# Optimization experiments

Hardware: AMD Instinct MI355X
Metric: run time of the kernel (lower is better)

Reference implementation:

```python
import jax, jax.numpy as jnp
import numpy as np

Q, C, D = 4096, 4096, 1024
EPS = 1e-6  # torch.nn.PairwiseDistance default eps, added to (x1 - x2)


def _cdist_l2(a, b):
    # ||(a + EPS) - b||_2 for all pairs, via GEMM formulation.
    a = a + EPS
    sq = (jnp.sum(a * a, axis=1)[:, None]
          + jnp.sum(b * b, axis=1)[None, :]
          - 2.0 * a @ b.T)
    return jnp.sqrt(jnp.maximum(sq, 0.0))


def setup_inputs() -> dict:
    key = jax.random.key(0)
    k1, k2, k3, k4, k5, k6 = jax.random.split(key, 6)
    return {
        "context_rgb_features": jax.random.normal(k1, (C, D), dtype=jnp.float32),
        "context_flow_features": jax.random.normal(k2, (C, D), dtype=jnp.float32),
        "target_rgb_features": jax.random.normal(k3, (Q, D), dtype=jnp.float32),
        "target_flow_features": jax.random.normal(k4, (Q, D), dtype=jnp.float32),
        "c_r": jax.random.uniform(k5, (Q,), dtype=jnp.float32, minval=0.1, maxval=1.0),
        "c_f": jax.random.uniform(k6, (Q,), dtype=jnp.float32, minval=0.1, maxval=1.0),
    }


def reference(context_rgb_features, context_flow_features,
              target_rgb_features, target_flow_features, c_r, c_f):
    denom = c_r + c_f
    w_r = (c_r / denom)[:, None]   # [Q, 1]
    w_f = (c_f / denom)[:, None]
    d_rgb = _cdist_l2(target_rgb_features, context_rgb_features)    # [Q, C]
    d_flow = _cdist_l2(target_flow_features, context_flow_features)  # [Q, C]
    posterior = w_r * jnp.exp(-d_rgb) + w_f * jnp.exp(-d_flow)
    return posterior / jnp.sum(posterior, axis=1, keepdims=True)
```

## Files before the change

### kernel.cpp

```cpp
#include <hip/hip_runtime.h>
#include <hip/hip_bf16.h>

#define QN 4096
#define CN 4096
#define DN 1024
#define EPSV 1e-6f

#define BM 128
#define BN 128
#define BK 64
#define TILE (BM * BK)

#define MATSZ ((size_t)QN * DN)

using bf16x8 = __attribute__((ext_vector_type(8))) __bf16;
using f32x4  = __attribute__((ext_vector_type(4))) float;

static __device__ __forceinline__ unsigned short f2bf_rne(float x) {
  unsigned int u = __float_as_uint(x);
  unsigned int r = (u + 0x7FFFu + ((u >> 16) & 1u)) >> 16;
  return (unsigned short)r;
}
static __device__ __forceinline__ float bf2f(unsigned short h) {
  return __uint_as_float(((unsigned int)h) << 16);
}

static __device__ __forceinline__ void gload_lds16(const unsigned short* g, unsigned short* l) {
  __builtin_amdgcn_global_load_lds(
      (const __attribute__((address_space(1))) unsigned int*)g,
      (__attribute__((address_space(3))) unsigned int*)l, 16, 0, 0);
}


__global__ void prep_kernel(const float* __restrict__ tgt_r, const float* __restrict__ tgt_f,
                            const float* __restrict__ ctx_r, const float* __restrict__ ctx_f,
                            unsigned short* __restrict__ ws16, float* __restrict__ norms) {
  const int row = blockIdx.x;
  const int mat = blockIdx.y;
  const int t = threadIdx.x;
  const float* src; float eps;
  switch (mat) {
    case 0:  src = tgt_r; eps = EPSV; break;
    case 1:  src = tgt_f; eps = EPSV; break;
    case 2:  src = ctx_r; eps = 0.f;  break;
    default: src = ctx_f; eps = 0.f;  break;
  }
  unsigned short* hi = ws16 + (size_t)mat * MATSZ;
  float* nrm = norms + (size_t)mat * QN;
  const size_t base = (size_t)row * DN;
  float4 v = ((const float4*)(src + base))[t];
  float a[4] = {v.x + eps, v.y + eps, v.z + eps, v.w + eps};
  float ss = 0.f;
  unsigned short hh[4];
#pragma unroll
  for (int k = 0; k < 4; ++k) {
    hh[k] = f2bf_rne(a[k]);
    float f = bf2f(hh[k]);
    ss += f * f;
  }
  ((ushort4*)(hi + base))[t] = make_ushort4(hh[0], hh[1], hh[2], hh[3]);

#pragma unroll
  for (int o = 32; o > 0; o >>= 1) ss += __shfl_down(ss, o);
  __shared__ float red[4];
  if ((t & 63) == 0) red[t >> 6] = ss;
  __syncthreads();
  if (t == 0) nrm[row] = red[0] + red[1] + red[2] + red[3];
}

template <bool ACCUM>
__global__ __launch_bounds__(256, 3)
void gemm_kernel(const unsigned short* __restrict__ A,
                 const unsigned short* __restrict__ B,
                 const float* __restrict__ tn,
                 const float* __restrict__ cn,
                 const float* __restrict__ cw_num,
                 const float* __restrict__ cw_oth,
                 float* __restrict__ out) {
  __shared__ unsigned short S[2 * TILE];

  const int t = threadIdx.x;
  const int lane = t & 63;
  const int wid = t >> 6;
  const int wr = wid >> 1;
  const int wc = wid & 1;
  const int row0 = blockIdx.y * BM;
  const int col0 = blockIdx.x * BN;

  f32x4 acc[4][4];
#pragma unroll
  for (int i = 0; i < 4; ++i)
#pragma unroll
    for (int j = 0; j < 4; ++j)
      acc[i][j] = (f32x4){0.f, 0.f, 0.f, 0.f};

  const int srw = lane >> 3;
  const int sch = (lane & 7) ^ srw;
  const size_t src_off = (size_t)(wid * 8 + srw) * DN + sch * 8;
  const size_t aoff = (size_t)row0 * DN + src_off;
  const size_t boff = (size_t)col0 * DN + src_off;
  unsigned short* ldsW = S + wid * 8 * BK;

  const unsigned short* pA = A + aoff;
  const unsigned short* pB = B + boff;

  const int lr = lane & 15;
  const int lq = lane >> 4;
  const int sc0 = (lq ^ (lr & 7)) * 8;
  int ra[4], rb[4];
#pragma unroll
  for (int i = 0; i < 4; ++i) {
    ra[i] = (wr * 64 + i * 16 + lr) * BK + sc0;
    rb[i] = (wc * 64 + i * 16 + lr) * BK + sc0;
  }
#define KS1(x) ((x) ^ 32)

  for (int kc = 0; kc < DN / BK; ++kc) {
    const int k = kc * BK;
    __syncthreads();
#pragma unroll
    for (int it = 0; it < 4; ++it) {
      const size_t g = (size_t)it * 32 * DN + k;
      unsigned short* l = ldsW + it * 32 * BK;
      gload_lds16(pA + g, l + 0 * TILE);
      gload_lds16(pB + g, l + 1 * TILE);
    }
    __syncthreads();

#pragma unroll
    for (int ksub = 0; ksub < 2; ++ksub) {
      bf16x8 ar[4], br[4];
#pragma unroll
      for (int i = 0; i < 4; ++i) {
        const int oa = ksub ? KS1(ra[i]) : ra[i];
        const int ob = ksub ? KS1(rb[i]) : rb[i];
        ar[i] = *(const bf16x8*)(S + oa);
        br[i] = *(const bf16x8*)(S + TILE + ob);
      }
#pragma unroll
      for (int i = 0; i < 4; ++i)
#pragma unroll
        for (int j = 0; j < 4; ++j)
          acc[i][j] = __builtin_amdgcn_mfma_f32_16x16x32_bf16(ar[i], br[j], acc[i][j], 0, 0, 0);
    }
  }

  float cnv[4];
  int ccv[4];
#pragma unroll
  for (int j = 0; j < 4; ++j) {
    ccv[j] = col0 + wc * 64 + j * 16 + lr;
    cnv[j] = cn[ccv[j]];
  }

#pragma unroll
  for (int i = 0; i < 4; ++i) {
#pragma unroll
    for (int r = 0; r < 4; ++r) {
      const int tq = row0 + wr * 64 + i * 16 + lq * 4 + r;
      const float tnq = tn[tq];
      const float num = cw_num[tq], oth = cw_oth[tq];
      const float wgt = num / (num + oth);
      float* orow = out + (size_t)tq * CN;
#pragma unroll
      for (int j = 0; j < 4; ++j) {
        const float sq = tnq + cnv[j] - 2.f * acc[i][j][r];
        const float d = sqrtf(fmaxf(sq, 0.f));
        const float e = wgt * __expf(-d);
        if (ACCUM) {
          orow[ccv[j]] += e;
        } else {
          orow[ccv[j]] = e;
        }
      }
    }
  }
}

__global__ void norm_kernel(float* __restrict__ out) {
  const int row = blockIdx.x;
  const int t = threadIdx.x;
  float4* p = (float4*)(out + (size_t)row * CN);
  float4 v[4];
  float s = 0.f;
#pragma unroll
  for (int i = 0; i < 4; ++i) {
    v[i] = p[t + 256 * i];
    s += v[i].x + v[i].y + v[i].z + v[i].w;
  }
#pragma unroll
  for (int o = 32; o > 0; o >>= 1) s += __shfl_down(s, o);
  __shared__ float red[4];
  if ((t & 63) == 0) red[t >> 6] = s;
  __syncthreads();
  const float inv = 1.f / (red[0] + red[1] + red[2] + red[3]);
#pragma unroll
  for (int i = 0; i < 4; ++i) {
    v[i].x *= inv; v[i].y *= inv; v[i].z *= inv; v[i].w *= inv;
    p[t + 256 * i] = v[i];
  }
}

extern "C" void kernel_launch(void* const* d_in, const int* in_sizes, int n_in,
                              void* d_out, int out_size, void* d_ws, size_t ws_size,
                              hipStream_t stream) {
  const float* ctx_r = (const float*)d_in[0];
  const float* ctx_f = (const float*)d_in[1];
  const float* tgt_r = (const float*)d_in[2];
  const float* tgt_f = (const float*)d_in[3];
  const float* c_r   = (const float*)d_in[4];
  const float* c_f   = (const float*)d_in[5];
  float* out = (float*)d_out;
  unsigned short* ws16 = (unsigned short*)d_ws;
  float* norms = (float*)(ws16 + 4 * MATSZ);

  prep_kernel<<<dim3(QN, 4), 256, 0, stream>>>(tgt_r, tgt_f, ctx_r, ctx_f, ws16, norms);
  gemm_kernel<false><<<dim3(CN / BN, QN / BM), 256, 0, stream>>>(
      ws16 + 0 * MATSZ, ws16 + 2 * MATSZ, norms, norms + 2 * QN, c_r, c_f, out);
  gemm_kernel<true><<<dim3(CN / BN, QN / BM), 256, 0, stream>>>(
      ws16 + 1 * MATSZ, ws16 + 3 * MATSZ, norms + QN, norms + 3 * QN, c_f, c_r, out);
  norm_kernel<<<QN, 256, 0, stream>>>(out);
}
```

Measured before the change: 226.5 us.

## Fuse RGB and flow GEMMs into one kernel with LDS-staged coalesced epilogue

The two separate GEMM launches (RGB, then flow with read-modify-write accumulation into the output) become one kernel that loads all four bf16 operand tiles and keeps two accumulator sets. The combined posterior is written once, which removes the second kernel's read of the output matrix. The epilogue stages results through LDS so each row segment is stored as contiguous float4 writes. The prep and norm kernels now give one wavefront per row and drop the shared-memory reductions. The cost is double the accumulator registers and LDS, and occupancy drops from 3 to 2 blocks per CU.

```diff
diff --git a/kernel.cpp b/kernel.cpp
--- a/kernel.cpp
+++ b/kernel.cpp
@@ -12,6 +12,7 @@
 #define TILE (BM * BK)
 
 #define MATSZ ((size_t)QN * DN)
+#define SFP 132
 
 using bf16x8 = __attribute__((ext_vector_type(8))) __bf16;
 using f32x4  = __attribute__((ext_vector_type(4))) float;
@@ -35,9 +36,11 @@
 __global__ void prep_kernel(const float* __restrict__ tgt_r, const float* __restrict__ tgt_f,
                             const float* __restrict__ ctx_r, const float* __restrict__ ctx_f,
                             unsigned short* __restrict__ ws16, float* __restrict__ norms) {
-  const int row = blockIdx.x;
+  const int t = threadIdx.x;
+  const int w = t >> 6;
+  const int lane = t & 63;
+  const int row = blockIdx.x * 4 + w;
   const int mat = blockIdx.y;
-  const int t = threadIdx.x;
   const float* src; float eps;
   switch (mat) {
     case 0:  src = tgt_r; eps = EPSV; break;
@@ -48,36 +51,33 @@
   unsigned short* hi = ws16 + (size_t)mat * MATSZ;
   float* nrm = norms + (size_t)mat * QN;
   const size_t base = (size_t)row * DN;
-  float4 v = ((const float4*)(src + base))[t];
-  float a[4] = {v.x + eps, v.y + eps, v.z + eps, v.w + eps};
+  const float4* s4 = (const float4*)(src + base);
+  ushort4* d4 = (ushort4*)(hi + base);
   float ss = 0.f;
-  unsigned short hh[4];
-#pragma unroll
-  for (int k = 0; k < 4; ++k) {
-    hh[k] = f2bf_rne(a[k]);
-    float f = bf2f(hh[k]);
-    ss += f * f;
-  }
-  ((ushort4*)(hi + base))[t] = make_ushort4(hh[0], hh[1], hh[2], hh[3]);
-
+#pragma unroll
+  for (int i = 0; i < 4; ++i) {
+    float4 v = s4[lane + 64 * i];
+    float a[4] = {v.x + eps, v.y + eps, v.z + eps, v.w + eps};
+    unsigned short hh[4];
+#pragma unroll
+    for (int k = 0; k < 4; ++k) {
+      hh[k] = f2bf_rne(a[k]);
+      float f = bf2f(hh[k]);
+      ss += f * f;
+    }
+    d4[lane + 64 * i] = make_ushort4(hh[0], hh[1], hh[2], hh[3]);
+  }
 #pragma unroll
   for (int o = 32; o > 0; o >>= 1) ss += __shfl_down(ss, o);
-  __shared__ float red[4];
-  if ((t & 63) == 0) red[t >> 6] = ss;
-  __syncthreads();
-  if (t == 0) nrm[row] = red[0] + red[1] + red[2] + red[3];
-}
-
-template <bool ACCUM>
-__global__ __launch_bounds__(256, 3)
-void gemm_kernel(const unsigned short* __restrict__ A,
-                 const unsigned short* __restrict__ B,
-                 const float* __restrict__ tn,
-                 const float* __restrict__ cn,
-                 const float* __restrict__ cw_num,
-                 const float* __restrict__ cw_oth,
+  if (lane == 0) nrm[row] = ss;
+}
+
+__global__ __launch_bounds__(256, 2)
+void gemm_kernel(const unsigned short* __restrict__ ws16,
+                 const float* __restrict__ norms,
+                 const float* __restrict__ c_r, const float* __restrict__ c_f,
                  float* __restrict__ out) {
-  __shared__ unsigned short S[2 * TILE];
+  __shared__ unsigned short S[4 * TILE];
 
   const int t = threadIdx.x;
   const int lane = t & 63;
@@ -87,12 +87,14 @@
   const int row0 = blockIdx.y * BM;
   const int col0 = blockIdx.x * BN;
 
-  f32x4 acc[4][4];
-#pragma unroll
-  for (int i = 0; i < 4; ++i)
-#pragma unroll
-    for (int j = 0; j < 4; ++j)
-      acc[i][j] = (f32x4){0.f, 0.f, 0.f, 0.f};
+  f32x4 acc[2][4][4];
+#pragma unroll
+  for (int m = 0; m < 2; ++m)
+#pragma unroll
+    for (int i = 0; i < 4; ++i)
+#pragma unroll
+      for (int j = 0; j < 4; ++j)
+        acc[m][i][j] = (f32x4){0.f, 0.f, 0.f, 0.f};
 
   const int srw = lane >> 3;
   const int sch = (lane & 7) ^ srw;
@@ -101,8 +103,10 @@
   const size_t boff = (size_t)col0 * DN + src_off;
   unsigned short* ldsW = S + wid * 8 * BK;
 
-  const unsigned short* pA = A + aoff;
-  const unsigned short* pB = B + boff;
+  const unsigned short* pAr = ws16 + 0 * MATSZ + aoff;
+  const unsigned short* pAf = ws16 + 1 * MATSZ + aoff;
+  const unsigned short* pBr = ws16 + 2 * MATSZ + boff;
+  const unsigned short* pBf = ws16 + 3 * MATSZ + boff;
 
   const int lr = lane & 15;
   const int lq = lane >> 4;
@@ -122,82 +126,107 @@
     for (int it = 0; it < 4; ++it) {
       const size_t g = (size_t)it * 32 * DN + k;
       unsigned short* l = ldsW + it * 32 * BK;
-      gload_lds16(pA + g, l + 0 * TILE);
-      gload_lds16(pB + g, l + 1 * TILE);
+      gload_lds16(pAr + g, l + 0 * TILE);
+      gload_lds16(pAf + g, l + 1 * TILE);
+      gload_lds16(pBr + g, l + 2 * TILE);
+      gload_lds16(pBf + g, l + 3 * TILE);
     }
     __syncthreads();
 
 #pragma unroll
     for (int ksub = 0; ksub < 2; ++ksub) {
-      bf16x8 ar[4], br[4];
+      bf16x8 ar[4], af[4], br[4], bf[4];
 #pragma unroll
       for (int i = 0; i < 4; ++i) {
         const int oa = ksub ? KS1(ra[i]) : ra[i];
         const int ob = ksub ? KS1(rb[i]) : rb[i];
-        ar[i] = *(const bf16x8*)(S + oa);
-        br[i] = *(const bf16x8*)(S + TILE + ob);
+        ar[i] = *(const bf16x8*)(S + 0 * TILE + oa);
+        af[i] = *(const bf16x8*)(S + 1 * TILE + oa);
+        br[i] = *(const bf16x8*)(S + 2 * TILE + ob);
+        bf[i] = *(const bf16x8*)(S + 3 * TILE + ob);
       }
 #pragma unroll
       for (int i = 0; i < 4; ++i)
 #pragma unroll
-        for (int j = 0; j < 4; ++j)
-          acc[i][j] = __builtin_amdgcn_mfma_f32_16x16x32_bf16(ar[i], br[j], acc[i][j], 0, 0, 0);
-    }
-  }
-
-  float cnv[4];
-  int ccv[4];
+        for (int j = 0; j < 4; ++j) {
+          acc[0][i][j] = __builtin_amdgcn_mfma_f32_16x16x32_bf16(ar[i], br[j], acc[0][i][j], 0, 0, 0);
+          acc[1][i][j] = __builtin_amdgcn_mfma_f32_16x16x32_bf16(af[i], bf[j], acc[1][i][j], 0, 0, 0);
+        }
+    }
+  }
+
+  const float* tn_r = norms;
+  const float* tn_f = norms + QN;
+  const float* cn_r = norms + 2 * QN;
+  const float* cn_f = norms + 3 * QN;
+
+  float cnr[4], cnf[4];
 #pragma unroll
   for (int j = 0; j < 4; ++j) {
-    ccv[j] = col0 + wc * 64 + j * 16 + lr;
-    cnv[j] = cn[ccv[j]];
-  }
+    const int cc = col0 + wc * 64 + j * 16 + lr;
+    cnr[j] = cn_r[cc];
+    cnf[j] = cn_f[cc];
+  }
+
+  float* Sf = (float*)S;
+  const int lrow = t >> 3;
+  const int c0 = (t & 7) * 16;
+  const int grow_base = row0 + (lrow >> 4) * 64 + (lrow & 15);
+
+  __syncthreads();
 
 #pragma unroll
   for (int i = 0; i < 4; ++i) {
+    if (i > 0) __syncthreads();
 #pragma unroll
     for (int r = 0; r < 4; ++r) {
       const int tq = row0 + wr * 64 + i * 16 + lq * 4 + r;
-      const float tnq = tn[tq];
-      const float num = cw_num[tq], oth = cw_oth[tq];
-      const float wgt = num / (num + oth);
-      float* orow = out + (size_t)tq * CN;
+      const float tnr = tn_r[tq];
+      const float tnf = tn_f[tq];
+      const float cr = c_r[tq], cf = c_f[tq];
+      const float inv = 1.f / (cr + cf);
+      const float wgr = cr * inv, wgf = cf * inv;
+      float* sfrow = Sf + (wr * 16 + lq * 4 + r) * SFP + wc * 64 + lr;
 #pragma unroll
       for (int j = 0; j < 4; ++j) {
-        const float sq = tnq + cnv[j] - 2.f * acc[i][j][r];
-        const float d = sqrtf(fmaxf(sq, 0.f));
-        const float e = wgt * __expf(-d);
-        if (ACCUM) {
-          orow[ccv[j]] += e;
-        } else {
-          orow[ccv[j]] = e;
-        }
+        const float sr_ = tnr + cnr[j] - 2.f * acc[0][i][j][r];
+        const float sf_ = tnf + cnf[j] - 2.f * acc[1][i][j][r];
+        const float dr = sqrtf(fmaxf(sr_, 0.f));
+        const float df = sqrtf(fmaxf(sf_, 0.f));
+        sfrow[j * 16] = wgr * __expf(-dr) + wgf * __expf(-df);
       }
     }
+    __syncthreads();
+    const float* src = Sf + lrow * SFP + c0;
+    float4 v0 = ((const float4*)src)[0];
+    float4 v1 = ((const float4*)src)[1];
+    float4 v2 = ((const float4*)src)[2];
+    float4 v3 = ((const float4*)src)[3];
+    float4* dst = (float4*)(out + (size_t)(grow_base + i * 16) * CN + col0 + c0);
+    dst[0] = v0; dst[1] = v1; dst[2] = v2; dst[3] = v3;
   }
 }
 
 __global__ void norm_kernel(float* __restrict__ out) {
-  const int row = blockIdx.x;
   const int t = threadIdx.x;
+  const int w = t >> 6;
+  const int lane = t & 63;
+  const int row = blockIdx.x * 4 + w;
   float4* p = (float4*)(out + (size_t)row * CN);
-  float4 v[4];
+  float4 v[16];
   float s = 0.f;
 #pragma unroll
-  for (int i = 0; i < 4; ++i) {
-    v[i] = p[t + 256 * i];
+  for (int i = 0; i < 16; ++i) {
+    v[i] = p[lane + 64 * i];
     s += v[i].x + v[i].y + v[i].z + v[i].w;
   }
 #pragma unroll
   for (int o = 32; o > 0; o >>= 1) s += __shfl_down(s, o);
-  __shared__ float red[4];
-  if ((t & 63) == 0) red[t >> 6] = s;
-  __syncthreads();
-  const float inv = 1.f / (red[0] + red[1] + red[2] + red[3]);
-#pragma unroll
-  for (int i = 0; i < 4; ++i) {
+  const float inv = 1.f / __shfl(s, 0);
+#pragma unroll
+  for (int i = 0; i < 16; ++i) {
     v[i].x *= inv; v[i].y *= inv; v[i].z *= inv; v[i].w *= inv;
-    p[t + 256 * i] = v[i];
+    p[lane + 64 * i] = v[i];
   }
 }
 
@@ -214,10 +243,7 @@
   unsigned short* ws16 = (unsigned short*)d_ws;
   float* norms = (float*)(ws16 + 4 * MATSZ);
 
-  prep_kernel<<<dim3(QN, 4), 256, 0, stream>>>(tgt_r, tgt_f, ctx_r, ctx_f, ws16, norms);
-  gemm_kernel<false><<<dim3(CN / BN, QN / BM), 256, 0, stream>>>(
-      ws16 + 0 * MATSZ, ws16 + 2 * MATSZ, norms, norms + 2 * QN, c_r, c_f, out);
-  gemm_kernel<true><<<dim3(CN / BN, QN / BM), 256, 0, stream>>>(
-      ws16 + 1 * MATSZ, ws16 + 3 * MATSZ, norms + QN, norms + 3 * QN, c_f, c_r, out);
-  norm_kernel<<<QN, 256, 0, stream>>>(out);
-}
+  prep_kernel<<<dim3(QN / 4, 4), 256, 0, stream>>>(tgt_r, tgt_f, ctx_r, ctx_f, ws16, norms);
+  gemm_kernel<<<dim3(CN / BN, QN / BM), 256, 0, stream>>>(ws16, norms, c_r, c_f, out);
+  norm_kernel<<<QN / 4, 256, 0, stream>>>(out);
+}
```

New measurement: 236.0 us. +4.2%, slower.

## Fuse rgb and flow GEMMs into one double-buffered kernel

Applied to the files above, without the earlier changes.

Merges the two separate distance GEMM launches into a single kernel that accumulates both the rgb and flow products per output tile and writes the combined posterior once. This removes the read-modify-write pass over the output from the second GEMM and one launch. The main loop is restructured to a K=32 tile with double-buffered LDS staging, so the next tile loads while the current one computes. The cost is twice the accumulator registers, with launch bounds lowered to 2 blocks per CU, which reduces occupancy.

```diff
diff --git a/kernel.cpp b/kernel.cpp
--- a/kernel.cpp
+++ b/kernel.cpp
@@ -8,8 +8,9 @@
 
 #define BM 128
 #define BN 128
-#define BK 64
-#define TILE (BM * BK)
+#define TK 32
+#define TILEK (BM * TK)
+#define NT (DN / TK)
 
 #define MATSZ ((size_t)QN * DN)
 
@@ -59,7 +60,6 @@
     ss += f * f;
   }
   ((ushort4*)(hi + base))[t] = make_ushort4(hh[0], hh[1], hh[2], hh[3]);
-
 #pragma unroll
   for (int o = 32; o > 0; o >>= 1) ss += __shfl_down(ss, o);
   __shared__ float red[4];
@@ -68,16 +68,12 @@
   if (t == 0) nrm[row] = red[0] + red[1] + red[2] + red[3];
 }
 
-template <bool ACCUM>
-__global__ __launch_bounds__(256, 3)
-void gemm_kernel(const unsigned short* __restrict__ A,
-                 const unsigned short* __restrict__ B,
-                 const float* __restrict__ tn,
-                 const float* __restrict__ cn,
-                 const float* __restrict__ cw_num,
-                 const float* __restrict__ cw_oth,
+__global__ __launch_bounds__(256, 2)
+void gemm_kernel(const unsigned short* __restrict__ ws16,
+                 const float* __restrict__ norms,
+                 const float* __restrict__ c_r, const float* __restrict__ c_f,
                  float* __restrict__ out) {
-  __shared__ unsigned short S[2 * TILE];
+  __shared__ unsigned short S[2 * 4 * TILEK];
 
   const int t = threadIdx.x;
   const int lane = t & 63;
@@ -87,91 +83,102 @@
   const int row0 = blockIdx.y * BM;
   const int col0 = blockIdx.x * BN;
 
-  f32x4 acc[4][4];
-#pragma unroll
-  for (int i = 0; i < 4; ++i)
-#pragma unroll
-    for (int j = 0; j < 4; ++j)
-      acc[i][j] = (f32x4){0.f, 0.f, 0.f, 0.f};
-
-  const int srw = lane >> 3;
-  const int sch = (lane & 7) ^ srw;
-  const size_t src_off = (size_t)(wid * 8 + srw) * DN + sch * 8;
-  const size_t aoff = (size_t)row0 * DN + src_off;
-  const size_t boff = (size_t)col0 * DN + src_off;
-  unsigned short* ldsW = S + wid * 8 * BK;
-
-  const unsigned short* pA = A + aoff;
-  const unsigned short* pB = B + boff;
+  f32x4 acc[2][4][4];
+#pragma unroll
+  for (int m = 0; m < 2; ++m)
+#pragma unroll
+    for (int i = 0; i < 4; ++i)
+#pragma unroll
+      for (int j = 0; j < 4; ++j)
+        acc[m][i][j] = (f32x4){0.f, 0.f, 0.f, 0.f};
+
+  const int sch = ((lane & 3) ^ ((lane >> 3) & 3)) * 8;
+  const int r0 = wid * 16 + (lane >> 2);
+  const size_t sr0 = (size_t)r0 * DN + sch;
+  const size_t sr1 = (size_t)(r0 + 64) * DN + sch;
+  const int ldsb0 = (wid * 64) * 8;
+  const int ldsb1 = (256 + wid * 64) * 8;
+
+  const unsigned short* pAr = ws16 + 0 * MATSZ + (size_t)row0 * DN;
+  const unsigned short* pAf = ws16 + 1 * MATSZ + (size_t)row0 * DN;
+  const unsigned short* pBr = ws16 + 2 * MATSZ + (size_t)col0 * DN;
+  const unsigned short* pBf = ws16 + 3 * MATSZ + (size_t)col0 * DN;
 
   const int lr = lane & 15;
   const int lq = lane >> 4;
-  const int sc0 = (lq ^ (lr & 7)) * 8;
+  const int fch = (lq ^ ((lr >> 1) & 3)) * 8;
   int ra[4], rb[4];
 #pragma unroll
   for (int i = 0; i < 4; ++i) {
-    ra[i] = (wr * 64 + i * 16 + lr) * BK + sc0;
-    rb[i] = (wc * 64 + i * 16 + lr) * BK + sc0;
-  }
-#define KS1(x) ((x) ^ 32)
-
-  for (int kc = 0; kc < DN / BK; ++kc) {
-    const int k = kc * BK;
+    ra[i] = (wr * 64 + i * 16 + lr) * TK + fch;
+    rb[i] = (wc * 64 + i * 16 + lr) * TK + fch;
+  }
+
+#define STAGE(buf, kk)                                                        \
+  do {                                                                        \
+    unsigned short* Sb_ = S + (buf) * 4 * TILEK;                              \
+    gload_lds16(pAr + (kk) + sr0, Sb_ + 0 * TILEK + ldsb0);                   \
+    gload_lds16(pAr + (kk) + sr1, Sb_ + 0 * TILEK + ldsb1);                   \
+    gload_lds16(pAf + (kk) + sr0, Sb_ + 1 * TILEK + ldsb0);                   \
+    gload_lds16(pAf + (kk) + sr1, Sb_ + 1 * TILEK + ldsb1);                   \
+    gload_lds16(pBr + (kk) + sr0, Sb_ + 2 * TILEK + ldsb0);                   \
+    gload_lds16(pBr + (kk) + sr1, Sb_ + 2 * TILEK + ldsb1);                   \
+    gload_lds16(pBf + (kk) + sr0, Sb_ + 3 * TILEK + ldsb0);                   \
+    gload_lds16(pBf + (kk) + sr1, Sb_ + 3 * TILEK + ldsb1);                   \
+  } while (0)
+
+  STAGE(0, 0);
+  __syncthreads();
+
+  int cur = 0;
+  for (int tt = 0; tt < NT; ++tt) {
+    if (tt + 1 < NT) STAGE(cur ^ 1, (tt + 1) * TK);
+
+    const unsigned short* Sb = S + cur * 4 * TILEK;
+    bf16x8 ar[4], af[4], br[4], bf[4];
+#pragma unroll
+    for (int i = 0; i < 4; ++i) {
+      ar[i] = *(const bf16x8*)(Sb + 0 * TILEK + ra[i]);
+      af[i] = *(const bf16x8*)(Sb + 1 * TILEK + ra[i]);
+      br[i] = *(const bf16x8*)(Sb + 2 * TILEK + rb[i]);
+      bf[i] = *(const bf16x8*)(Sb + 3 * TILEK + rb[i]);
+    }
+#pragma unroll
+    for (int i = 0; i < 4; ++i)
+#pragma unroll
+      for (int j = 0; j < 4; ++j) {
+        acc[0][i][j] = __builtin_amdgcn_mfma_f32_16x16x32_bf16(ar[i], br[j], acc[0][i][j], 0, 0, 0);
+        acc[1][i][j] = __builtin_amdgcn_mfma_f32_16x16x32_bf16(af[i], bf[j], acc[1][i][j], 0, 0, 0);
+      }
+
     __syncthreads();
-#pragma unroll
-    for (int it = 0; it < 4; ++it) {
-      const size_t g = (size_t)it * 32 * DN + k;
-      unsigned short* l = ldsW + it * 32 * BK;
-      gload_lds16(pA + g, l + 0 * TILE);
-      gload_lds16(pB + g, l + 1 * TILE);
-    }
-    __syncthreads();
-
-#pragma unroll
-    for (int ksub = 0; ksub < 2; ++ksub) {
-      bf16x8 ar[4], br[4];
-#pragma unroll
-      for (int i = 0; i < 4; ++i) {
-        const int oa = ksub ? KS1(ra[i]) : ra[i];
-        const int ob = ksub ? KS1(rb[i]) : rb[i];
-        ar[i] = *(const bf16x8*)(S + oa);
-        br[i] = *(const bf16x8*)(S + TILE + ob);
-      }
-#pragma unroll
-      for (int i = 0; i < 4; ++i)
-#pragma unroll
-        for (int j = 0; j < 4; ++j)
-          acc[i][j] = __builtin_amdgcn_mfma_f32_16x16x32_bf16(ar[i], br[j], acc[i][j], 0, 0, 0);
-    }
-  }
-
-  float cnv[4];
-  int ccv[4];
-#pragma unroll
-  for (int j = 0; j < 4; ++j) {
-    ccv[j] = col0 + wc * 64 + j * 16 + lr;
-    cnv[j] = cn[ccv[j]];
-  }
+    cur ^= 1;
+  }
+
+  const float* tn_r = norms;
+  const float* tn_f = norms + QN;
+  const float* cn_r = norms + 2 * QN;
+  const float* cn_f = norms + 3 * QN;
 
 #pragma unroll
   for (int i = 0; i < 4; ++i) {
 #pragma unroll
     for (int r = 0; r < 4; ++r) {
       const int tq = row0 + wr * 64 + i * 16 + lq * 4 + r;
-      const float tnq = tn[tq];
-      const float num = cw_num[tq], oth = cw_oth[tq];
-      const float wgt = num / (num + oth);
-      float* orow = out + (size_t)tq * CN;
+      const float tnr = tn_r[tq];
+      const float tnf = tn_f[tq];
+      const float cr = c_r[tq], cf = c_f[tq];
+      const float inv = 1.f / (cr + cf);
+      const float wgr = cr * inv, wgf = cf * inv;
 #pragma unroll
       for (int j = 0; j < 4; ++j) {
-        const float sq = tnq + cnv[j] - 2.f * acc[i][j][r];
-        const float d = sqrtf(fmaxf(sq, 0.f));
-        const float e = wgt * __expf(-d);
-        if (ACCUM) {
-          orow[ccv[j]] += e;
-        } else {
-          orow[ccv[j]] = e;
-        }
+        const int cc = col0 + wc * 64 + j * 16 + lr;
+        const float sr_ = tnr + cn_r[cc] - 2.f * acc[0][i][j][r];
+        const float sf_ = tnf + cn_f[cc] - 2.f * acc[1][i][j][r];
+        const float dr = sqrtf(fmaxf(sr_, 0.f));
+        const float df = sqrtf(fmaxf(sf_, 0.f));
+        const float p = wgr * __expf(-dr) + wgf * __expf(-df);
+        out[(size_t)tq * CN + cc] = p;
       }
     }
   }
@@ -215,9 +222,6 @@
   float* norms = (float*)(ws16 + 4 * MATSZ);
 
   prep_kernel<<<dim3(QN, 4), 256, 0, stream>>>(tgt_r, tgt_f, ctx_r, ctx_f, ws16, norms);
-  gemm_kernel<false><<<dim3(CN / BN, QN / BM), 256, 0, stream>>>(
-      ws16 + 0 * MATSZ, ws16 + 2 * MATSZ, norms, norms + 2 * QN, c_r, c_f, out);
-  gemm_kernel<true><<<dim3(CN / BN, QN / BM), 256, 0, stream>>>(
-      ws16 + 1 * MATSZ, ws16 + 3 * MATSZ, norms + QN, norms + 3 * QN, c_f, c_r, out);
+  gemm_kernel<<<dim3(CN / BN, QN / BM), 256, 0, stream>>>(ws16, norms, c_r, c_f, out);
   norm_kernel<<<QN, 256, 0, stream>>>(out);
 }
```

Result: slower. 232.3 us (+2.5%).

## Enlarge GEMM tiles to 256x256 with 8 waves and double-buffered LDS

Applied to the files above, without the earlier changes.

The GEMM block tile grows from 128x128 to 256x256 and uses 512 threads. Each wave now computes a 128x64 sub-tile. Global-to-LDS loads for the next K slice are issued into a second LDS buffer while MFMAs run on the current one, so one barrier per iteration replaces two. This raises arithmetic intensity and overlaps load latency with compute. In exchange it uses more registers and LDS (64KB) and launches only 256 blocks, which may limit occupancy and cause wave-quantization effects.

```diff
diff --git a/kernel.cpp b/kernel.cpp
--- a/kernel.cpp
+++ b/kernel.cpp
@@ -6,10 +6,12 @@
 #define DN 1024
 #define EPSV 1e-6f
 
-#define BM 128
-#define BN 128
-#define BK 64
-#define TILE (BM * BK)
+#define BM 256
+#define BN 256
+#define TK 64
+#define NT (DN / TK)
+#define ATILE (BM * TK)
+#define BUFE (2 * ATILE)
 
 #define MATSZ ((size_t)QN * DN)
 
@@ -59,7 +61,6 @@
     ss += f * f;
   }
   ((ushort4*)(hi + base))[t] = make_ushort4(hh[0], hh[1], hh[2], hh[3]);
-
 #pragma unroll
   for (int o = 32; o > 0; o >>= 1) ss += __shfl_down(ss, o);
   __shared__ float red[4];
@@ -69,7 +70,7 @@
 }
 
 template <bool ACCUM>
-__global__ __launch_bounds__(256, 3)
+__global__ __launch_bounds__(512, 2)
 void gemm_kernel(const unsigned short* __restrict__ A,
                  const unsigned short* __restrict__ B,
                  const float* __restrict__ tn,
@@ -77,101 +78,104 @@
                  const float* __restrict__ cw_num,
                  const float* __restrict__ cw_oth,
                  float* __restrict__ out) {
-  __shared__ unsigned short S[2 * TILE];
+  __shared__ unsigned short S[2 * BUFE];
 
   const int t = threadIdx.x;
   const int lane = t & 63;
   const int wid = t >> 6;
-  const int wr = wid >> 1;
-  const int wc = wid & 1;
+  const int wr = wid >> 2;
+  const int wc = wid & 3;
   const int row0 = blockIdx.y * BM;
   const int col0 = blockIdx.x * BN;
 
-  f32x4 acc[4][4];
-#pragma unroll
-  for (int i = 0; i < 4; ++i)
-#pragma unroll
-    for (int j = 0; j < 4; ++j)
-      acc[i][j] = (f32x4){0.f, 0.f, 0.f, 0.f};
+  f32x4 acc[8][4];
+#pragma unroll
+  for (int m = 0; m < 8; ++m)
+#pragma unroll
+    for (int n = 0; n < 4; ++n)
+      acc[m][n] = (f32x4){0.f, 0.f, 0.f, 0.f};
 
   const int srw = lane >> 3;
   const int sch = (lane & 7) ^ srw;
   const size_t src_off = (size_t)(wid * 8 + srw) * DN + sch * 8;
-  const size_t aoff = (size_t)row0 * DN + src_off;
-  const size_t boff = (size_t)col0 * DN + src_off;
-  unsigned short* ldsW = S + wid * 8 * BK;
-
-  const unsigned short* pA = A + aoff;
-  const unsigned short* pB = B + boff;
+  const int ldsw = wid * 512;
+
+  const unsigned short* pA = A + (size_t)row0 * DN + src_off;
+  const unsigned short* pB = B + (size_t)col0 * DN + src_off;
 
   const int lr = lane & 15;
   const int lq = lane >> 4;
   const int sc0 = (lq ^ (lr & 7)) * 8;
-  int ra[4], rb[4];
-#pragma unroll
-  for (int i = 0; i < 4; ++i) {
-    ra[i] = (wr * 64 + i * 16 + lr) * BK + sc0;
-    rb[i] = (wc * 64 + i * 16 + lr) * BK + sc0;
-  }
+  int ra[8], rb[4];
+#pragma unroll
+  for (int m = 0; m < 8; ++m) ra[m] = (wr * 128 + m * 16 + lr) * TK + sc0;
+#pragma unroll
+  for (int n = 0; n < 4; ++n) rb[n] = (wc * 64 + n * 16 + lr) * TK + sc0;
 #define KS1(x) ((x) ^ 32)
 
-  for (int kc = 0; kc < DN / BK; ++kc) {
-    const int k = kc * BK;
+#define STAGE(buf, kk)                                                        \
+  do {                                                                        \
+    unsigned short* Sb_ = S + (buf) * BUFE;                                   \
+    _Pragma("unroll")                                                         \
+    for (int i_ = 0; i_ < 4; ++i_) {                                          \
+      const size_t g_ = (size_t)i_ * 64 * DN + (kk);                          \
+      gload_lds16(pA + g_, Sb_ + i_ * 4096 + ldsw);                           \
+      gload_lds16(pB + g_, Sb_ + ATILE + i_ * 4096 + ldsw);                   \
+    }                                                                         \
+  } while (0)
+
+  STAGE(0, 0);
+  __syncthreads();
+
+  int cur = 0;
+  for (int tt = 0; tt < NT; ++tt) {
+    if (tt + 1 < NT) STAGE(cur ^ 1, (tt + 1) * TK);
+
+    const unsigned short* Sb = S + cur * BUFE;
+#pragma unroll
+    for (int ksub = 0; ksub < 2; ++ksub) {
+      bf16x8 a[8], b[4];
+#pragma unroll
+      for (int m = 0; m < 8; ++m)
+        a[m] = *(const bf16x8*)(Sb + (ksub ? KS1(ra[m]) : ra[m]));
+#pragma unroll
+      for (int n = 0; n < 4; ++n)
+        b[n] = *(const bf16x8*)(Sb + ATILE + (ksub ? KS1(rb[n]) : rb[n]));
+#pragma unroll
+      for (int m = 0; m < 8; ++m)
+#pragma unroll
+        for (int n = 0; n < 4; ++n)
+          acc[m][n] = __builtin_amdgcn_mfma_f32_16x16x32_bf16(a[m], b[n], acc[m][n], 0, 0, 0);
+    }
+
     __syncthreads();
-#pragma unroll
-    for (int it = 0; it < 4; ++it) {
-      const size_t g = (size_t)it * 32 * DN + k;
-      unsigned short* l = ldsW + it * 32 * BK;
-      gload_lds16(pA + g, l + 0 * TILE);
-      gload_lds16(pB + g, l + 1 * TILE);
-    }
-    __syncthreads();
-
-#pragma unroll
-    for (int ksub = 0; ksub < 2; ++ksub) {
-      bf16x8 ar[4], br[4];
-#pragma unroll
-      for (int i = 0; i < 4; ++i) {
-        const int oa = ksub ? KS1(ra[i]) : ra[i];
-        const int ob = ksub ? KS1(rb[i]) : rb[i];
-        ar[i] = *(const bf16x8*)(S + oa);
-        br[i] = *(const bf16x8*)(S + TILE + ob);
-      }
-#pragma unroll
-      for (int i = 0; i < 4; ++i)
-#pragma unroll
-        for (int j = 0; j < 4; ++j)
-          acc[i][j] = __builtin_amdgcn_mfma_f32_16x16x32_bf16(ar[i], br[j], acc[i][j], 0, 0, 0);
-    }
+    cur ^= 1;
   }
 
   float cnv[4];
   int ccv[4];
 #pragma unroll
-  for (int j = 0; j < 4; ++j) {
-    ccv[j] = col0 + wc * 64 + j * 16 + lr;
-    cnv[j] = cn[ccv[j]];
-  }
-
-#pragma unroll
-  for (int i = 0; i < 4; ++i) {
+  for (int n = 0; n < 4; ++n) {
+    ccv[n] = col0 + wc * 64 + n * 16 + lr;
+    cnv[n] = cn[ccv[n]];
+  }
+
+#pragma unroll
+  for (int m = 0; m < 8; ++m) {
 #pragma unroll
     for (int r = 0; r < 4; ++r) {
-      const int tq = row0 + wr * 64 + i * 16 + lq * 4 + r;
+      const int tq = row0 + wr * 128 + m * 16 + lq * 4 + r;
       const float tnq = tn[tq];
       const float num = cw_num[tq], oth = cw_oth[tq];
       const float wgt = num / (num + oth);
       float* orow = out + (size_t)tq * CN;
 #pragma unroll
-      for (int j = 0; j < 4; ++j) {
-        const float sq = tnq + cnv[j] - 2.f * acc[i][j][r];
+      for (int n = 0; n < 4; ++n) {
+        const float sq = tnq + cnv[n] - 2.f * acc[m][n][r];
         const float d = sqrtf(fmaxf(sq, 0.f));
         const float e = wgt * __expf(-d);
-        if (ACCUM) {
-          orow[ccv[j]] += e;
-        } else {
-          orow[ccv[j]] = e;
-        }
+        if (ACCUM) orow[ccv[n]] += e;
+        else       orow[ccv[n]] = e;
       }
     }
   }
@@ -215,9 +219,9 @@
   float* norms = (float*)(ws16 + 4 * MATSZ);
 
   prep_kernel<<<dim3(QN, 4), 256, 0, stream>>>(tgt_r, tgt_f, ctx_r, ctx_f, ws16, norms);
-  gemm_kernel<false><<<dim3(CN / BN, QN / BM), 256, 0, stream>>>(
+  gemm_kernel<false><<<dim3(CN / BN, QN / BM), 512, 0, stream>>>(
       ws16 + 0 * MATSZ, ws16 + 2 * MATSZ, norms, norms + 2 * QN, c_r, c_f, out);
-  gemm_kernel<true><<<dim3(CN / BN, QN / BM), 256, 0, stream>>>(
+  gemm_kernel<true><<<dim3(CN / BN, QN / BM), 512, 0, stream>>>(
       ws16 + 1 * MATSZ, ws16 + 3 * MATSZ, norms + QN, norms + 3 * QN, c_f, c_r, out);
   norm_kernel<<<QN, 256, 0, stream>>>(out);
 }
```

Measured after the change: 231.5 us. 2.2% more time.
